# Optimization experiments

Measured on AMD Instinct MI355X. Metric: run time of the kernel, lower is better.

Reference implementation:

```python
import jax, jax.numpy as jnp
import numpy as np

GAMMA = 0.7
WALK_LEN = 3
TAU = 1.0
N_FILTERS = 8


def _row_norm(A):
    return A / jnp.clip(jnp.sum(A, axis=-1, keepdims=True), 1e-12, None)


def _motif_channel(A, idx, Wadj, gates):
    # A: [n,n]; idx: [I,k] int node indices; Wadj: [F,k,k]; gates: [L]
    n = A.shape[0]
    I, k = idx.shape
    F = Wadj.shape[0]
    # learnable filter adjacency: softplus, symmetrize, zero diagonal, row-normalize
    S = jax.nn.softplus(Wadj)
    S = 0.5 * (S + jnp.swapaxes(S, -1, -2)) * (1.0 - jnp.eye(k, dtype=A.dtype))
    Sf = _row_norm(S)                                  # [F,k,k]
    # per-instance induced subgraph transition matrices
    As = A[idx[:, :, None], idx[:, None, :]]           # [I,k,k]
    Tm = _row_norm(As)                                 # [I,k,k]
    # batched Kronecker product: Km[i,f,a*k+b,c*k+d] = Tm[i,a,c]*Sf[f,b,d]
    Km = (Tm[:, None, :, None, :, None] * Sf[None, :, None, :, None, :]).reshape(I, F, k * k, k * k)
    gp = jax.nn.softplus(gates)                        # [L] length gates
    M = Km
    acc = (GAMMA * gp[0]) * jnp.trace(M, axis1=-2, axis2=-1)   # [I,F]
    for p in range(2, WALK_LEN + 1):
        M = M @ Km
        acc = acc + (GAMMA ** p * gp[p - 1]) * jnp.trace(M, axis1=-2, axis2=-1)
    sims = acc                                         # [I,F] RWK similarities
    alphas = jax.nn.softmax(sims / max(1e-06, TAU), axis=-1)
    contrib = (alphas * sims) / float(k)               # [I,F]
    upd = jnp.broadcast_to(contrib[:, None, :], (I, k, F)).reshape(I * k, F)
    return jnp.zeros((n, F), A.dtype).at[idx.reshape(-1)].add(upd)


def _layer(A, tri_idx, cyc_idx, H, Wt, Wc, g, lng, lnb, w1, b1, w2, b2):
    Phi = jnp.concatenate([_motif_channel(A, tri_idx, Wt, g),
                           _motif_channel(A, cyc_idx, Wc, g),
                           H], axis=1)                 # [n, in_ch]
    mu = jnp.mean(Phi, axis=-1, keepdims=True)
    var = jnp.var(Phi, axis=-1, keepdims=True)
    X = (Phi - mu) / jnp.sqrt(var + 1e-5) * lng + lnb  # LayerNorm
    return jax.nn.gelu(X @ w1 + b1, approximate=False) @ w2 + b2  # dropout = identity (eval)


def _templates():
    tri = np.zeros((3, 3), np.float32)
    for u, v in [(0, 1), (1, 2), (0, 2)]:
        tri[u, v] = tri[v, u] = 1.0
    cyc = np.zeros((4, 4), np.float32)
    for u, v in [(0, 1), (1, 2), (2, 3), (3, 0)]:
        cyc[u, v] = cyc[v, u] = 1.0
    return tri, cyc


def setup_inputs() -> dict:
    key = jax.random.key(0)
    ks = jax.random.split(key, 16)
    n, D, HID = 4096, 128, 128
    A = (jax.random.uniform(ks[0], (n, n)) < 0.01).astype(jnp.float32)
    A = 0.5 * (A + A.T)
    A = A * (1.0 - jnp.eye(n, dtype=jnp.float32))
    tri_idx = jax.random.randint(ks[1], (30000, 3), 0, n, dtype=jnp.int32)
    cyc_idx = jax.random.randint(ks[2], (15000, 4), 0, n, dtype=jnp.int32)
    tri_t, cyc_t = _templates()
    def w_adj(k, tmpl):
        return jnp.asarray(tmpl)[None] + 0.05 * jax.random.normal(k, (N_FILTERS,) + tmpl.shape, dtype=jnp.float32)
    in0, in1 = 17, 145
    inp = {"A_full": A, "tri_idx": tri_idx, "cyc_idx": cyc_idx,
           "W_tri_0": w_adj(ks[3], tri_t), "W_cyc_0": w_adj(ks[4], cyc_t),
           "gates_0": jnp.zeros((WALK_LEN,), jnp.float32),
           "lng_0": jnp.ones((in0,), jnp.float32), "lnb_0": jnp.zeros((in0,), jnp.float32),
           "w1_0": 0.05 * jax.random.normal(ks[5], (in0, HID), jnp.float32), "b1_0": jnp.zeros((HID,), jnp.float32),
           "w2_0": 0.05 * jax.random.normal(ks[6], (HID, D), jnp.float32), "b2_0": jnp.zeros((D,), jnp.float32),
           "W_tri_1": w_adj(ks[7], tri_t), "W_cyc_1": w_adj(ks[8], cyc_t),
           "gates_1": jnp.zeros((WALK_LEN,), jnp.float32),
           "lng_1": jnp.ones((in1,), jnp.float32), "lnb_1": jnp.zeros((in1,), jnp.float32),
           "w1_1": 0.05 * jax.random.normal(ks[9], (in1, HID), jnp.float32), "b1_1": jnp.zeros((HID,), jnp.float32),
           "w2_1": 0.05 * jax.random.normal(ks[10], (HID, D), jnp.float32), "b2_1": jnp.zeros((D,), jnp.float32)}
    return inp


def reference(A_full, tri_idx, cyc_idx,
              W_tri_0, W_cyc_0, gates_0, lng_0, lnb_0, w1_0, b1_0, w2_0, b2_0,
              W_tri_1, W_cyc_1, gates_1, lng_1, lnb_1, w1_1, b1_1, w2_1, b2_1):
    # base channel (use_base=True): node degree from dense adjacency
    H = jnp.sum(A_full, axis=-1, keepdims=True)        # [n,1]
    Z = _layer(A_full, tri_idx, cyc_idx, H, W_tri_0, W_cyc_0, gates_0, lng_0, lnb_0, w1_0, b1_0, w2_0, b2_0)
    H = jnp.concatenate([Z, H], axis=1)                # residual_cat: [n,129]
    Z = _layer(A_full, tri_idx, cyc_idx, H, W_tri_1, W_cyc_1, gates_1, lng_1, lnb_1, w1_1, b1_1, w2_1, b2_1)
    H = jnp.concatenate([Z, H], axis=1)                # [n,257]
    return H
```

## Files before the change

### kernel.cpp

```cpp
#include <hip/hip_runtime.h>
#include <math.h>
#include <stdint.h>

#define GAMMA 0.7f
#define CAP 96

typedef __attribute__((ext_vector_type(8))) short short8v;
typedef __attribute__((ext_vector_type(4))) float f32x4;

__device__ __forceinline__ float sp_dev(float x) {
    return fmaxf(x, 0.0f) + log1pf(expf(-fabsf(x)));
}
__device__ __forceinline__ float gelu_exact(float x) {
    return 0.5f * x * (1.0f + erff(x * 0.70710678118654752f));
}
__device__ __forceinline__ uint16_t f2bf(float x) {
    union { float f; uint32_t u; } c; c.f = x;
    uint32_t u = c.u + 0x7FFFu + ((c.u >> 16) & 1u);
    return (uint16_t)(u >> 16);
}

__global__ void prep_kernel(const float* __restrict__ Wt0, const float* __restrict__ Wc0,
                            const float* __restrict__ g0,
                            const float* __restrict__ Wt1, const float* __restrict__ Wc1,
                            const float* __restrict__ g1,
                            const float* __restrict__ w1_0, const float* __restrict__ w2_0,
                            const float* __restrict__ w1_1, const float* __restrict__ w2_1,
                            float* __restrict__ dcoef,
                            uint16_t* __restrict__ Wb10, uint16_t* __restrict__ Wb20,
                            uint16_t* __restrict__ Wb11, uint16_t* __restrict__ Wb21,
                            int* __restrict__ cursor, int ncur) {
    int tid = threadIdx.x;
    int gtid = blockIdx.x * blockDim.x + tid;
    int stride = gridDim.x * blockDim.x;

    for (int i = gtid; i < ncur; i += stride) cursor[i] = 0;

    if (blockIdx.x == 0 && tid < 32) {
        int L = tid >> 4, m = (tid >> 3) & 1, f = tid & 7;
        int k = m ? 4 : 3;
        const float* W = L ? (m ? Wc1 : Wt1) : (m ? Wc0 : Wt0);
        const float* g = L ? g1 : g0;
        float S[4][4], Y[4][4];
        for (int a = 0; a < k; a++)
            for (int b = 0; b < k; b++)
                S[a][b] = sp_dev(W[(f * k + a) * k + b]);
        for (int a = 0; a < k; a++)
            for (int b = 0; b < k; b++)
                Y[a][b] = (a == b) ? 0.0f : 0.5f * (S[a][b] + S[b][a]);
        for (int a = 0; a < k; a++) {
            float rs = 0.0f;
            for (int b = 0; b < k; b++) rs += Y[a][b];
            rs = fmaxf(rs, 1e-12f);
            for (int b = 0; b < k; b++) Y[a][b] /= rs;
        }
        float t1 = 0, t2 = 0, t3 = 0;
        for (int a = 0; a < k; a++) t1 += Y[a][a];
        for (int a = 0; a < k; a++)
            for (int b = 0; b < k; b++) t2 += Y[a][b] * Y[b][a];
        for (int a = 0; a < k; a++)
            for (int b = 0; b < k; b++)
                for (int c = 0; c < k; c++) t3 += Y[a][b] * Y[b][c] * Y[c][a];
        float* d = dcoef + ((L * 2 + m) * 8 + f) * 3;
        d[0] = GAMMA * sp_dev(g[0]) * t1;
        d[1] = GAMMA * GAMMA * sp_dev(g[1]) * t2;
        d[2] = GAMMA * GAMMA * GAMMA * sp_dev(g[2]) * t3;
    }
    for (int idx = gtid; idx < 57344; idx += stride) {
        if (idx < 4096) {
            int c = idx >> 5, k = idx & 31;
            Wb10[idx] = (k < 17) ? f2bf(w1_0[k * 128 + c]) : 0;
        } else if (idx < 20480) {
            int e = idx - 4096; int c = e >> 7, k = e & 127;
            Wb20[e] = f2bf(w2_0[k * 128 + c]);
        } else if (idx < 40960) {
            int e = idx - 20480; int c = e / 160, k = e % 160;
            Wb11[e] = (k < 145) ? f2bf(w1_1[k * 128 + c]) : 0;
        } else {
            int e = idx - 40960; int c = e >> 7, k = e & 127;
            Wb21[e] = f2bf(w2_1[k * 128 + c]);
        }
    }
}

__global__ void rowsum_kernel(const float* __restrict__ A, int n,
                              float* __restrict__ H0, float* __restrict__ out) {
    int row = blockIdx.x;
    const float4* Arow = (const float4*)(A + (size_t)row * n);
    int n4 = n >> 2;
    float s = 0.0f;
    for (int i = threadIdx.x; i < n4; i += blockDim.x) {
        float4 v = Arow[i];
        s += v.x + v.y + v.z + v.w;
    }
    __shared__ float red[4];
    for (int off = 32; off > 0; off >>= 1) s += __shfl_down(s, off);
    if ((threadIdx.x & 63) == 0) red[threadIdx.x >> 6] = s;
    __syncthreads();
    if (threadIdx.x == 0) {
        float t = red[0] + red[1] + red[2] + red[3];
        H0[row] = t;
        out[(size_t)row * 257 + 256] = t;
    }
}

template <int K>
__device__ __forceinline__ void contrib_body(
    const float* __restrict__ A, int n, const int* __restrict__ idx, int I, int i,
    const float (*dc)[8][3], float* __restrict__ cont,
    int* __restrict__ cursor, int* __restrict__ slotbuf) {
    int nodes[K];
#pragma unroll
    for (int j = 0; j < K; j++) nodes[j] = idx[i * K + j];

    float Tm[K][K];
#pragma unroll
    for (int a = 0; a < K; a++) {
        float rs = 0.0f;
#pragma unroll
        for (int b = 0; b < K; b++) {
            float v = A[(size_t)nodes[a] * n + nodes[b]];
            Tm[a][b] = v; rs += v;
        }
        rs = fmaxf(rs, 1e-12f);
        float inv = 1.0f / rs;
#pragma unroll
        for (int b = 0; b < K; b++) Tm[a][b] *= inv;
    }
    float t1 = 0, t2 = 0, t3 = 0;
#pragma unroll
    for (int a = 0; a < K; a++) t1 += Tm[a][a];
#pragma unroll
    for (int a = 0; a < K; a++)
#pragma unroll
        for (int b = 0; b < K; b++) t2 += Tm[a][b] * Tm[b][a];
#pragma unroll
    for (int a = 0; a < K; a++)
#pragma unroll
        for (int b = 0; b < K; b++) {
            float ab = Tm[a][b];
#pragma unroll
            for (int c = 0; c < K; c++) t3 += ab * Tm[b][c] * Tm[c][a];
        }
#pragma unroll
    for (int L = 0; L < 2; L++) {
        float sims[8], mx = -1e30f;
#pragma unroll
        for (int f = 0; f < 8; f++) {
            sims[f] = dc[L][f][0] * t1 + dc[L][f][1] * t2 + dc[L][f][2] * t3;
            mx = fmaxf(mx, sims[f]);
        }
        float es[8], se = 0.0f;
#pragma unroll
        for (int f = 0; f < 8; f++) { es[f] = expf(sims[f] - mx); se += es[f]; }
        float inv = 1.0f / se;
        float* cp = cont + ((size_t)L * I + i) * 8;
#pragma unroll
        for (int f = 0; f < 8; f++) cp[f] = es[f] * inv * sims[f] * (1.0f / (float)K);
    }
#pragma unroll
    for (int j = 0; j < K; j++) {
        int v = nodes[j];
        int pos = atomicAdd(&cursor[v], 1);
        if (pos < CAP) slotbuf[(size_t)v * CAP + pos] = i;
    }
}

__global__ void contrib_fused_kernel(const float* __restrict__ A, int n,
                                     const int* __restrict__ tri, int Itri,
                                     const int* __restrict__ cyc, int Icyc, int B3,
                                     const float* __restrict__ dcoef,
                                     float* __restrict__ tri_c, float* __restrict__ cyc_c,
                                     int* __restrict__ cursor, int* __restrict__ slotbuf) {
    __shared__ float dc[2][8][3];
    int tid = threadIdx.x;
    bool isTri = (int)blockIdx.x < B3;
    const float* dcL0 = dcoef + (isTri ? 0 : 24);
    const float* dcL1 = dcoef + (isTri ? 48 : 72);
    if (tid < 24) dc[0][tid / 3][tid % 3] = dcL0[tid];
    else if (tid < 48) { int t = tid - 24; dc[1][t / 3][t % 3] = dcL1[t]; }
    __syncthreads();

    if (isTri) {
        int i = blockIdx.x * 256 + tid;
        if (i < Itri)
            contrib_body<3>(A, n, tri, Itri, i, dc, tri_c, cursor, slotbuf);
    } else {
        int i = (blockIdx.x - B3) * 256 + tid;
        if (i < Icyc)
            contrib_body<4>(A, n, cyc, Icyc, i, dc, cyc_c, cursor + n,
                            slotbuf + (size_t)n * CAP);
    }
}

__global__ __launch_bounds__(512) void mega_kernel(
    const float* __restrict__ tri_c, int Itri,
    const float* __restrict__ cyc_c, int Icyc,
    const int* __restrict__ cursor, const int* __restrict__ slotbuf,
    const float* __restrict__ H0,
    const float* __restrict__ lng0, const float* __restrict__ lnb0,
    const uint16_t* __restrict__ Wb10, const float* __restrict__ b1_0,
    const uint16_t* __restrict__ Wb20, const float* __restrict__ b2_0,
    const float* __restrict__ lng1, const float* __restrict__ lnb1,
    const uint16_t* __restrict__ Wb11, const float* __restrict__ b1_1,
    const uint16_t* __restrict__ Wb21, const float* __restrict__ b2_1,
    float* __restrict__ out, int n) {
    __shared__ uint16_t Xs[16][168];
    __shared__ uint16_t Hs[16][136];
    __shared__ float    Zs[16][129];
    __shared__ float    phi0[16][17];
    __shared__ float    f1[16][16];
    __shared__ float    h0s[16];

    int tid = threadIdx.x;
    int v0 = blockIdx.x * 16;
    int wave = tid >> 6;
    int lane = tid & 63;
    int lr = lane & 15, lg = lane >> 4;

    {
        int r = tid >> 5;
        int combo = tid & 31;
        int m = combo >> 4, L = (combo >> 3) & 1, f = combo & 7;
        int v = v0 + r;
        int cnt = cursor[m * n + v];
        cnt = cnt < CAP ? cnt : CAP;
        const int* bucket = slotbuf + ((size_t)(m * n + v)) * CAP;
        const float* c = m ? cyc_c : tri_c;
        int I = m ? Icyc : Itri;
        float sum = 0.0f;
        for (int j = 0; j < cnt; j++) {
            int i = bucket[j];
            sum += c[((size_t)L * I + i) * 8 + f];
        }
        if (L == 0) phi0[r][m * 8 + f] = sum;
        else        f1[r][m * 8 + f] = sum;
        if (combo == 0) { float h = H0[v]; phi0[r][16] = h; h0s[r] = h; }
    }
    __syncthreads();

    {
        int r = tid >> 5;
        int j = tid & 31;
        float x = (j < 17) ? phi0[r][j] : 0.0f;
        float s1 = x, s2 = x * x;
        for (int o = 16; o > 0; o >>= 1) { s1 += __shfl_xor(s1, o); s2 += __shfl_xor(s2, o); }
        float mu = s1 / 17.0f;
        float rstd = rsqrtf(s2 / 17.0f - mu * mu + 1e-5f);
        Xs[r][j] = (j < 17) ? f2bf((x - mu) * rstd * lng0[j] + lnb0[j]) : (uint16_t)0;
    }
    __syncthreads();

    {
        int col = wave * 16 + lr;
        f32x4 acc = {0.f, 0.f, 0.f, 0.f};
        short8v a = *(const short8v*)&Xs[lr][lg * 8];
        short8v b = *(const short8v*)(Wb10 + (size_t)col * 32 + lg * 8);
        acc = __builtin_amdgcn_mfma_f32_16x16x32_bf16(a, b, acc, 0, 0, 0);
        float bias = b1_0[col];
#pragma unroll
        for (int i = 0; i < 4; i++)
            Hs[lg * 4 + i][col] = f2bf(gelu_exact(acc[i] + bias));
    }
    __syncthreads();

    {
        int col = wave * 16 + lr;
        f32x4 acc = {0.f, 0.f, 0.f, 0.f};
#pragma unroll
        for (int ks = 0; ks < 4; ks++) {
            short8v a = *(const short8v*)&Hs[lr][ks * 32 + lg * 8];
            short8v b = *(const short8v*)(Wb20 + (size_t)col * 128 + ks * 32 + lg * 8);
            acc = __builtin_amdgcn_mfma_f32_16x16x32_bf16(a, b, acc, 0, 0, 0);
        }
        float bias = b2_0[col];
#pragma unroll
        for (int i = 0; i < 4; i++) {
            int row = lg * 4 + i;
            float val = acc[i] + bias;
            out[(size_t)(v0 + row) * 257 + 128 + col] = val;
            Zs[row][col] = val;
        }
    }
    __syncthreads();

    {
        int rr = tid >> 5;
        int t = tid & 31;
        float ph[5];
        float s1 = 0.0f, s2 = 0.0f;
#pragma unroll
        for (int s = 0; s < 5; s++) {
            int j = t + 32 * s;
            float x = 0.0f;
            if (j < 16) x = f1[rr][j];
            else if (j < 144) x = Zs[rr][j - 16];
            else if (j == 144) x = h0s[rr];
            ph[s] = x;
            if (j < 145) { s1 += x; s2 += x * x; }
        }
        for (int o = 16; o > 0; o >>= 1) { s1 += __shfl_xor(s1, o); s2 += __shfl_xor(s2, o); }
        float mu = s1 / 145.0f;
        float rstd = rsqrtf(s2 / 145.0f - mu * mu + 1e-5f);
#pragma unroll
        for (int s = 0; s < 5; s++) {
            int j = t + 32 * s;
            Xs[rr][j] = (j < 145) ? f2bf((ph[s] - mu) * rstd * lng1[j] + lnb1[j]) : (uint16_t)0;
        }
    }
    __syncthreads();

    {
        int col = wave * 16 + lr;
        f32x4 acc = {0.f, 0.f, 0.f, 0.f};
#pragma unroll
        for (int ks = 0; ks < 5; ks++) {
            short8v a = *(const short8v*)&Xs[lr][ks * 32 + lg * 8];
            short8v b = *(const short8v*)(Wb11 + (size_t)col * 160 + ks * 32 + lg * 8);
            acc = __builtin_amdgcn_mfma_f32_16x16x32_bf16(a, b, acc, 0, 0, 0);
        }
        float bias = b1_1[col];
#pragma unroll
        for (int i = 0; i < 4; i++)
            Hs[lg * 4 + i][col] = f2bf(gelu_exact(acc[i] + bias));
    }
    __syncthreads();

    {
        int col = wave * 16 + lr;
        f32x4 acc = {0.f, 0.f, 0.f, 0.f};
#pragma unroll
        for (int ks = 0; ks < 4; ks++) {
            short8v a = *(const short8v*)&Hs[lr][ks * 32 + lg * 8];
            short8v b = *(const short8v*)(Wb21 + (size_t)col * 128 + ks * 32 + lg * 8);
            acc = __builtin_amdgcn_mfma_f32_16x16x32_bf16(a, b, acc, 0, 0, 0);
        }
        float bias = b2_1[col];
#pragma unroll
        for (int i = 0; i < 4; i++) {
            int row = lg * 4 + i;
            out[(size_t)(v0 + row) * 257 + col] = acc[i] + bias;
        }
    }
}

extern "C" void kernel_launch(void* const* d_in, const int* in_sizes, int n_in,
                              void* d_out, int out_size, void* d_ws, size_t ws_size,
                              hipStream_t stream) {
    const float* A    = (const float*)d_in[0];
    const int*   tri  = (const int*)d_in[1];
    const int*   cyc  = (const int*)d_in[2];
    const float* Wt0  = (const float*)d_in[3];
    const float* Wc0  = (const float*)d_in[4];
    const float* g0   = (const float*)d_in[5];
    const float* lng0 = (const float*)d_in[6];
    const float* lnb0 = (const float*)d_in[7];
    const float* w1_0 = (const float*)d_in[8];
    const float* b1_0 = (const float*)d_in[9];
    const float* w2_0 = (const float*)d_in[10];
    const float* b2_0 = (const float*)d_in[11];
    const float* Wt1  = (const float*)d_in[12];
    const float* Wc1  = (const float*)d_in[13];
    const float* g1   = (const float*)d_in[14];
    const float* lng1 = (const float*)d_in[15];
    const float* lnb1 = (const float*)d_in[16];
    const float* w1_1 = (const float*)d_in[17];
    const float* b1_1 = (const float*)d_in[18];
    const float* w2_1 = (const float*)d_in[19];
    const float* b2_1 = (const float*)d_in[20];

    int n    = out_size / 257;
    int Itri = in_sizes[1] / 3;
    int Icyc = in_sizes[2] / 4;

    float* ws    = (float*)d_ws;
    float* dcoef = ws;
    float* H0    = ws + 128;
    float* tri_c = H0 + n;
    float* cyc_c = tri_c + (size_t)2 * Itri * 8;
    int*   cursor  = (int*)(cyc_c + (size_t)2 * Icyc * 8);
    int*   slotbuf = cursor + (size_t)2 * n;
    uint16_t* Wb10 = (uint16_t*)(slotbuf + (size_t)2 * n * CAP);
    uint16_t* Wb20 = Wb10 + 128 * 32;
    uint16_t* Wb11 = Wb20 + 128 * 128;
    uint16_t* Wb21 = Wb11 + 128 * 160;
    float* out = (float*)d_out;

    prep_kernel<<<64, 256, 0, stream>>>(Wt0, Wc0, g0, Wt1, Wc1, g1,
                                        w1_0, w2_0, w1_1, w2_1,
                                        dcoef, Wb10, Wb20, Wb11, Wb21,
                                        cursor, 2 * n);

    rowsum_kernel<<<n, 256, 0, stream>>>(A, n, H0, out);

    int B3 = (Itri + 255) / 256;
    int B4 = (Icyc + 255) / 256;
    contrib_fused_kernel<<<B3 + B4, 256, 0, stream>>>(
        A, n, tri, Itri, cyc, Icyc, B3, dcoef, tri_c, cyc_c, cursor, slotbuf);

    mega_kernel<<<n / 16, 512, 0, stream>>>(
        tri_c, Itri, cyc_c, Icyc, cursor, slotbuf, H0,
        lng0, lnb0, Wb10, b1_0, Wb20, b2_0,
        lng1, lnb1, Wb11, b1_1, Wb21, b2_1, out, n);
}
```

Baseline: 77.05 us.

## Fuse rowsum into contrib kernel and split each motif instance across four lanes

Merges the row-sum (degree) kernel and the motif contribution kernel into one launch, with rowsum rows handled by extra blocks after the motif blocks. Each motif instance is now processed by a group of four lanes: each lane loads one row of the induced subgraph and shares it by shuffles, which spreads the scattered A loads across lanes and lets each lane write its contributions as a float2. Triangles are padded to 4x4 with an identity entry, and the traces are corrected by subtracting 1. This removes one kernel launch and lets the rowsum work overlap with the latency-bound gathers, at the cost of redundant 4x4 trace arithmetic on every lane.

```diff
diff --git a/kernel.cpp b/kernel.cpp
--- a/kernel.cpp
+++ b/kernel.cpp
@@ -83,65 +83,57 @@
     }
 }
 
-__global__ void rowsum_kernel(const float* __restrict__ A, int n,
-                              float* __restrict__ H0, float* __restrict__ out) {
-    int row = blockIdx.x;
-    const float4* Arow = (const float4*)(A + (size_t)row * n);
-    int n4 = n >> 2;
-    float s = 0.0f;
-    for (int i = threadIdx.x; i < n4; i += blockDim.x) {
-        float4 v = Arow[i];
-        s += v.x + v.y + v.z + v.w;
-    }
-    __shared__ float red[4];
-    for (int off = 32; off > 0; off >>= 1) s += __shfl_down(s, off);
-    if ((threadIdx.x & 63) == 0) red[threadIdx.x >> 6] = s;
-    __syncthreads();
-    if (threadIdx.x == 0) {
-        float t = red[0] + red[1] + red[2] + red[3];
-        H0[row] = t;
-        out[(size_t)row * 257 + 256] = t;
-    }
-}
-
 template <int K>
-__device__ __forceinline__ void contrib_body(
-    const float* __restrict__ A, int n, const int* __restrict__ idx, int I, int i,
+__device__ __forceinline__ void contrib_group(
+    const float* __restrict__ A, int n,
+    const int* __restrict__ idx, int I, int i, int g, int lane,
     const float (*dc)[8][3], float* __restrict__ cont,
     int* __restrict__ cursor, int* __restrict__ slotbuf) {
-    int nodes[K];
-#pragma unroll
-    for (int j = 0; j < K; j++) nodes[j] = idx[i * K + j];
-
-    float Tm[K][K];
-#pragma unroll
-    for (int a = 0; a < K; a++) {
-        float rs = 0.0f;
-#pragma unroll
-        for (int b = 0; b < K; b++) {
-            float v = A[(size_t)nodes[a] * n + nodes[b]];
-            Tm[a][b] = v; rs += v;
-        }
-        rs = fmaxf(rs, 1e-12f);
-        float inv = 1.0f / rs;
-#pragma unroll
-        for (int b = 0; b < K; b++) Tm[a][b] *= inv;
-    }
-    float t1 = 0, t2 = 0, t3 = 0;
-#pragma unroll
-    for (int a = 0; a < K; a++) t1 += Tm[a][a];
-#pragma unroll
-    for (int a = 0; a < K; a++)
-#pragma unroll
-        for (int b = 0; b < K; b++) t2 += Tm[a][b] * Tm[b][a];
-#pragma unroll
-    for (int a = 0; a < K; a++)
-#pragma unroll
-        for (int b = 0; b < K; b++) {
-            float ab = Tm[a][b];
-#pragma unroll
-            for (int c = 0; c < K; c++) t3 += ab * Tm[b][c] * Tm[c][a];
-        }
+    int base = lane & ~3;
+    int mynode = (g < K) ? idx[i * K + g] : 0;
+    int nb0 = __shfl(mynode, base + 0);
+    int nb1 = __shfl(mynode, base + 1);
+    int nb2 = __shfl(mynode, base + 2);
+    int nb3 = (K == 4) ? __shfl(mynode, base + 3) : 0;
+
+    float r0, r1, r2, r3;
+    if (K == 3) {
+        if (g < 3) {
+            const float* Ar = A + (size_t)mynode * n;
+            r0 = Ar[nb0]; r1 = Ar[nb1]; r2 = Ar[nb2]; r3 = 0.0f;
+        } else {
+            r0 = 0.0f; r1 = 0.0f; r2 = 0.0f; r3 = 1.0f;
+        }
+    } else {
+        const float* Ar = A + (size_t)mynode * n;
+        r0 = Ar[nb0]; r1 = Ar[nb1]; r2 = Ar[nb2]; r3 = Ar[nb3];
+    }
+    float rs = fmaxf(r0 + r1 + r2 + r3, 1e-12f);
+    float inv = 1.0f / rs;
+    r0 *= inv; r1 *= inv; r2 *= inv; r3 *= inv;
+
+    float M[4][4];
+#pragma unroll
+    for (int b = 0; b < 4; b++) {
+        M[b][0] = __shfl(r0, base + b);
+        M[b][1] = __shfl(r1, base + b);
+        M[b][2] = __shfl(r2, base + b);
+        M[b][3] = __shfl(r3, base + b);
+    }
+
+    float t1 = M[0][0] + M[1][1] + M[2][2] + M[3][3];
+    float t2 = 0.0f, t3 = 0.0f;
+#pragma unroll
+    for (int a = 0; a < 4; a++)
+#pragma unroll
+        for (int b = 0; b < 4; b++) {
+            float ab = M[a][b];
+            t2 += ab * M[b][a];
+#pragma unroll
+            for (int c = 0; c < 4; c++) t3 += ab * M[b][c] * M[c][a];
+        }
+    if (K == 3) { t1 -= 1.0f; t2 -= 1.0f; t3 -= 1.0f; }
+
 #pragma unroll
     for (int L = 0; L < 2; L++) {
         float sims[8], mx = -1e30f;
@@ -153,43 +145,73 @@
         float es[8], se = 0.0f;
 #pragma unroll
         for (int f = 0; f < 8; f++) { es[f] = expf(sims[f] - mx); se += es[f]; }
-        float inv = 1.0f / se;
-        float* cp = cont + ((size_t)L * I + i) * 8;
-#pragma unroll
-        for (int f = 0; f < 8; f++) cp[f] = es[f] * inv * sims[f] * (1.0f / (float)K);
-    }
-#pragma unroll
-    for (int j = 0; j < K; j++) {
-        int v = nodes[j];
-        int pos = atomicAdd(&cursor[v], 1);
-        if (pos < CAP) slotbuf[(size_t)v * CAP + pos] = i;
-    }
-}
-
-__global__ void contrib_fused_kernel(const float* __restrict__ A, int n,
-                                     const int* __restrict__ tri, int Itri,
-                                     const int* __restrict__ cyc, int Icyc, int B3,
-                                     const float* __restrict__ dcoef,
-                                     float* __restrict__ tri_c, float* __restrict__ cyc_c,
-                                     int* __restrict__ cursor, int* __restrict__ slotbuf) {
+        float sinv = 1.0f / se;
+        float cn[8];
+#pragma unroll
+        for (int f = 0; f < 8; f++) cn[f] = es[f] * sinv * sims[f] * (1.0f / (float)K);
+        float p0 = (g == 0) ? cn[0] : (g == 1) ? cn[2] : (g == 2) ? cn[4] : cn[6];
+        float p1 = (g == 0) ? cn[1] : (g == 1) ? cn[3] : (g == 2) ? cn[5] : cn[7];
+        float2 st = make_float2(p0, p1);
+        *(float2*)(cont + ((size_t)L * I + i) * 8 + 2 * g) = st;
+    }
+
+    if (g < K) {
+        int pos = atomicAdd(&cursor[mynode], 1);
+        if (pos < CAP) slotbuf[(size_t)mynode * CAP + pos] = i;
+    }
+}
+
+__global__ __launch_bounds__(256) void fused_kernel(
+    const float* __restrict__ A, int n,
+    const int* __restrict__ tri, int Itri,
+    const int* __restrict__ cyc, int Icyc,
+    int Btri, int Bcyc,
+    const float* __restrict__ dcoef,
+    float* __restrict__ tri_c, float* __restrict__ cyc_c,
+    int* __restrict__ cursor, int* __restrict__ slotbuf,
+    float* __restrict__ H0, float* __restrict__ out) {
     __shared__ float dc[2][8][3];
+    __shared__ float red[4];
+    int bid = blockIdx.x;
     int tid = threadIdx.x;
-    bool isTri = (int)blockIdx.x < B3;
-    const float* dcL0 = dcoef + (isTri ? 0 : 24);
-    const float* dcL1 = dcoef + (isTri ? 48 : 72);
-    if (tid < 24) dc[0][tid / 3][tid % 3] = dcL0[tid];
-    else if (tid < 48) { int t = tid - 24; dc[1][t / 3][t % 3] = dcL1[t]; }
-    __syncthreads();
-
-    if (isTri) {
-        int i = blockIdx.x * 256 + tid;
-        if (i < Itri)
-            contrib_body<3>(A, n, tri, Itri, i, dc, tri_c, cursor, slotbuf);
+
+    if (bid < Btri + Bcyc) {
+        bool isTri = bid < Btri;
+        const float* dl0 = dcoef + (isTri ? 0 : 24);
+        const float* dl1 = dcoef + (isTri ? 48 : 72);
+        if (tid < 24) dc[0][tid / 3][tid % 3] = dl0[tid];
+        else if (tid < 48) { int t = tid - 24; dc[1][t / 3][t % 3] = dl1[t]; }
+        __syncthreads();
+
+        int lane = tid & 63;
+        int g = tid & 3;
+        if (isTri) {
+            int i = bid * 64 + (tid >> 2);
+            if (i < Itri)
+                contrib_group<3>(A, n, tri, Itri, i, g, lane, dc, tri_c, cursor, slotbuf);
+        } else {
+            int i = (bid - Btri) * 64 + (tid >> 2);
+            if (i < Icyc)
+                contrib_group<4>(A, n, cyc, Icyc, i, g, lane, dc, cyc_c,
+                                 cursor + n, slotbuf + (size_t)n * CAP);
+        }
     } else {
-        int i = (blockIdx.x - B3) * 256 + tid;
-        if (i < Icyc)
-            contrib_body<4>(A, n, cyc, Icyc, i, dc, cyc_c, cursor + n,
-                            slotbuf + (size_t)n * CAP);
+        int row = bid - (Btri + Bcyc);
+        const float4* Arow = (const float4*)(A + (size_t)row * n);
+        int n4 = n >> 2;
+        float s = 0.0f;
+        for (int i = tid; i < n4; i += 256) {
+            float4 v = Arow[i];
+            s += v.x + v.y + v.z + v.w;
+        }
+        for (int off = 32; off > 0; off >>= 1) s += __shfl_down(s, off);
+        if ((tid & 63) == 0) red[tid >> 6] = s;
+        __syncthreads();
+        if (tid == 0) {
+            float t = red[0] + red[1] + red[2] + red[3];
+            H0[row] = t;
+            out[(size_t)row * 257 + 256] = t;
+        }
     }
 }
 
@@ -391,12 +413,11 @@
                                         dcoef, Wb10, Wb20, Wb11, Wb21,
                                         cursor, 2 * n);
 
-    rowsum_kernel<<<n, 256, 0, stream>>>(A, n, H0, out);
-
-    int B3 = (Itri + 255) / 256;
-    int B4 = (Icyc + 255) / 256;
-    contrib_fused_kernel<<<B3 + B4, 256, 0, stream>>>(
-        A, n, tri, Itri, cyc, Icyc, B3, dcoef, tri_c, cyc_c, cursor, slotbuf);
+    int Btri = (Itri + 63) / 64;
+    int Bcyc = (Icyc + 63) / 64;
+    fused_kernel<<<Btri + Bcyc + n, 256, 0, stream>>>(
+        A, n, tri, Itri, cyc, Icyc, Btri, Bcyc, dcoef,
+        tri_c, cyc_c, cursor, slotbuf, H0, out);
 
     mega_kernel<<<n / 16, 512, 0, stream>>>(
         tri_c, Itri, cyc_c, Icyc, cursor, slotbuf, H0,
```

Result: faster. 72.86 us (-5.4%).
